# Performance work log

Measured on AMD Instinct MI355X. Metric: run time of the kernel, lower is better.

The kernel has to match this reference:

```python
import jax, jax.numpy as jnp
import numpy as np

B, T, D = 8, 4096, 64

def setup_inputs() -> dict:
    key = jax.random.key(0)
    k1, k2 = jax.random.split(key)
    inputs = jax.random.normal(k1, (B, T, D), dtype=jnp.float32)
    # keras 'random_normal' initializer: stddev 0.05
    W = jax.random.normal(k2, (D, D), dtype=jnp.float32) * 0.05
    return {"inputs": inputs, "W": W}

def reference(inputs, W):
    # q = inputs @ W               : [B,T,D]
    # a = q @ inputs^T             : [B,T,T] (no scaling, bias b unused in original)
    # out = softmax(a, -1) @ inputs: [B,T,D]
    q = jnp.einsum('btd,de->bte', inputs, W)
    scores = jnp.einsum('btd,bsd->bts', q, inputs)
    attn = jax.nn.softmax(scores, axis=-1)
    return jnp.einsum('bts,bsd->btd', attn, inputs)
```

## Files before the change

### kernel.cpp

```cpp
#include <hip/hip_runtime.h>

typedef _Float16 f16;
typedef _Float16 f16x8 __attribute__((ext_vector_type(8)));
typedef __bf16 bf16x8 __attribute__((ext_vector_type(8)));
typedef float floatx4 __attribute__((ext_vector_type(4)));
typedef unsigned short u16;
typedef unsigned int u32;

#define B_N   8
#define T_SEQ 4096
#define DIM   64
#define NIT   32
#define FRAG  512
#define XSTR  72
#define LOG2E 1.44269504f

#if __has_builtin(__builtin_amdgcn_exp2f)
#define EXP2(x) __builtin_amdgcn_exp2f(x)
#else
#define EXP2(x) exp2f(x)
#endif

__device__ __forceinline__ uint4 xpose(uint2 p0, uint2 p1, int qd, int ln) {
  const int pos = qd & 1;
  u32 mx = pos ? p1.x : p0.x, my = pos ? p1.y : p0.y;
  u32 ox = pos ? p0.x : p1.x, oy = pos ? p0.y : p1.y;
  u32 tx = (u32)__shfl_xor((int)ox, 16, 64);
  u32 ty = (u32)__shfl_xor((int)oy, 16, 64);
  u32 lox = pos ? tx : mx, loy = pos ? ty : my;
  u32 hix = pos ? mx : tx, hiy = pos ? my : ty;
  const int src = ((2 * pos + (qd >> 1)) << 4) | ln;
  uint4 r;
  r.x = (u32)__shfl((int)lox, src, 64);
  r.y = (u32)__shfl((int)loy, src, 64);
  r.z = (u32)__shfl((int)hix, src, 64);
  r.w = (u32)__shfl((int)hiy, src, 64);
  return r;
}

__device__ __forceinline__ uint2 pack_bf4(floatx4 v) {
  __bf16 b0 = (__bf16)v[0], b1 = (__bf16)v[1], b2 = (__bf16)v[2], b3 = (__bf16)v[3];
  uint2 r;
  r.x = ((u32)__builtin_bit_cast(u16, b1) << 16) | __builtin_bit_cast(u16, b0);
  r.y = ((u32)__builtin_bit_cast(u16, b3) << 16) | __builtin_bit_cast(u16, b2);
  return r;
}
__device__ __forceinline__ uint2 pack_f16x4(floatx4 v, float sc) {
  f16 b0 = (f16)(v[0] * sc), b1 = (f16)(v[1] * sc), b2 = (f16)(v[2] * sc), b3 = (f16)(v[3] * sc);
  uint2 r;
  r.x = ((u32)__builtin_bit_cast(u16, b1) << 16) | __builtin_bit_cast(u16, b0);
  r.y = ((u32)__builtin_bit_cast(u16, b3) << 16) | __builtin_bit_cast(u16, b2);
  return r;
}

__launch_bounds__(256, 2)
__global__ void prep_kernel(const float* __restrict__ X,
                            u16* __restrict__ Kswz, u16* __restrict__ Vswz) {
  __shared__ __attribute__((aligned(16))) u16 Xs[DIM * XSTR];
  const int tid = threadIdx.x;
  const int lane = tid & 63, w = tid >> 6, qd = lane >> 4, ln = lane & 15;
  const int b = blockIdx.y, tx = blockIdx.x;
  const long xbase = ((long)b * T_SEQ + tx * 64) * DIM;

  {
    const int r = tid >> 2, c0 = (tid & 3) * 16;
    float v[16];
#pragma unroll
    for (int i = 0; i < 4; i++)
      *(float4*)&v[i * 4] = *(const float4*)(X + xbase + (long)r * DIM + c0 + i * 4);
    u16 h[16];
#pragma unroll
    for (int j = 0; j < 16; j++) h[j] = __builtin_bit_cast(u16, (f16)v[j]);
    *(uint4*)&Xs[r * XSTR + c0] = *(uint4*)&h[0];
    *(uint4*)&Xs[r * XSTR + c0 + 8] = *(uint4*)&h[8];
  }
  __syncthreads();

  {
    const long R = (long)b * (T_SEQ / 16) + tx * 4 + w;
#pragma unroll
    for (int ks = 0; ks < 2; ks++) {
      f16x8 kv = *(const f16x8*)&Xs[(w * 16 + ln) * XSTR + ks * 32 + qd * 8];
      *(f16x8*)(Kswz + (R * 2 + ks) * FRAG + lane * 8) = kv;
    }
  }
  {
    const long Cb = (long)b * 4 + w;
#pragma unroll
    for (int J = 0; J < 2; J++) {
      bf16x8 vv;
#pragma unroll
      for (int j = 0; j < 8; j++) {
        f16 hv = __builtin_bit_cast(f16, Xs[(J * 32 + qd * 8 + j) * XSTR + w * 16 + ln]);
        vv[j] = (__bf16)(float)hv;
      }
      *(bf16x8*)(Vswz + (Cb * (T_SEQ / 32) + tx * 2 + J) * FRAG + lane * 8) = vv;
    }
  }
}

__launch_bounds__(512, 4)
__global__ void attn_kernel(const u16* __restrict__ Kswz, const u16* __restrict__ Vswz,
                            const float* __restrict__ W, float* __restrict__ out) {
  __shared__ __attribute__((aligned(16))) float Opart[8][16][68];
  __shared__ float lpart[8][32];

  const int tid = threadIdx.x;
  const int lane = tid & 63, w = tid >> 6, qd = lane >> 4, ln = lane & 15;
  const int h = w >> 2;
  const int s = w & 3;
  const int bid = blockIdx.x;
  const int b = bid & 7;
  const int q0 = (bid >> 3) * 64;
  const long bbase = (long)b * T_SEQ * DIM;
  const long RB = (long)b * (T_SEQ / 16);

  f16x8 bXq[2][2];
#pragma unroll
  for (int rb = 0; rb < 2; rb++)
#pragma unroll
    for (int ks = 0; ks < 2; ks++)
      bXq[rb][ks] = *(const f16x8*)(Kswz +
          ((RB + (q0 >> 4) + h * 2 + rb) * 2 + ks) * FRAG + lane * 8);

  floatx4 accT[4][2];
#pragma unroll
  for (int eb = 0; eb < 4; eb++)
#pragma unroll
    for (int rb = 0; rb < 2; rb++) accT[eb][rb] = (floatx4)0.0f;
#pragma unroll
  for (int ks = 0; ks < 2; ks++)
#pragma unroll
    for (int eb = 0; eb < 4; eb++) {
      f16 tw[8];
#pragma unroll
      for (int j = 0; j < 8; j++)
        tw[j] = (f16)W[(ks * 32 + qd * 8 + j) * DIM + eb * 16 + ln];
      f16x8 aW = *(const f16x8*)tw;
#pragma unroll
      for (int rb = 0; rb < 2; rb++)
        accT[eb][rb] = __builtin_amdgcn_mfma_f32_16x16x32_f16(aW, bXq[rb][ks], accT[eb][rb], 0, 0, 0);
    }

  f16x8 bQ[2][2];
#pragma unroll
  for (int rb = 0; rb < 2; rb++)
#pragma unroll
    for (int ks = 0; ks < 2; ks++) {
      uint2 p0 = pack_f16x4(accT[ks * 2 + 0][rb], LOG2E);
      uint2 p1 = pack_f16x4(accT[ks * 2 + 1][rb], LOG2E);
      uint4 t = xpose(p0, p1, qd, ln);
      bQ[rb][ks] = __builtin_bit_cast(f16x8, t);
    }

  floatx4 O[4][2];
  float lacc[2] = {0.f, 0.f};
#pragma unroll
  for (int db = 0; db < 4; db++)
#pragma unroll
    for (int rb = 0; rb < 2; rb++) O[db][rb] = (floatx4)0.0f;

  const u16* pK = Kswz + (RB + s * 2) * 2 * FRAG + lane * 8;
  const u16* pV = Vswz + ((long)(b * 4) * (T_SEQ / 32) + s) * FRAG + lane * 8;

#pragma unroll 1
  for (int kt = 0; kt < NIT; kt++) {
    f16x8 kc[2][2];
#pragma unroll
    for (int ct = 0; ct < 2; ct++)
#pragma unroll
      for (int ks = 0; ks < 2; ks++)
        kc[ct][ks] = *(const f16x8*)(pK + (long)(kt * 16 + ct * 2 + ks) * FRAG);
    bf16x8 aV[4];
#pragma unroll
    for (int db = 0; db < 4; db++)
      aV[db] = *(const bf16x8*)(pV + ((long)db * (T_SEQ / 32) + kt * 4) * FRAG);

    floatx4 St[2][2];
#pragma unroll
    for (int ct = 0; ct < 2; ct++)
#pragma unroll
      for (int rb = 0; rb < 2; rb++) St[ct][rb] = (floatx4)0.0f;
#pragma unroll
    for (int ks = 0; ks < 2; ks++)
#pragma unroll
      for (int ct = 0; ct < 2; ct++)
#pragma unroll
        for (int rb = 0; rb < 2; rb++)
          St[ct][rb] = __builtin_amdgcn_mfma_f32_16x16x32_f16(kc[ct][ks], bQ[rb][ks], St[ct][rb], 0, 0, 0);

    bf16x8 bP[2];
#pragma unroll
    for (int rb = 0; rb < 2; rb++) {
      floatx4 e0, e1;
      float ps = 0.f;
#pragma unroll
      for (int r = 0; r < 4; r++) { e0[r] = EXP2(St[0][rb][r]); ps += e0[r]; }
#pragma unroll
      for (int r = 0; r < 4; r++) { e1[r] = EXP2(St[1][rb][r]); ps += e1[r]; }
      lacc[rb] += ps;
      bP[rb] = __builtin_bit_cast(bf16x8, xpose(pack_bf4(e0), pack_bf4(e1), qd, ln));
    }

#pragma unroll
    for (int db = 0; db < 4; db++)
#pragma unroll
      for (int rb = 0; rb < 2; rb++)
        O[db][rb] = __builtin_amdgcn_mfma_f32_16x16x32_bf16(aV[db], bP[rb], O[db][rb], 0, 0, 0);
  }

#pragma unroll
  for (int rb = 0; rb < 2; rb++) {
    float v = lacc[rb];
    v += __shfl_xor(v, 16, 64);
    v += __shfl_xor(v, 32, 64);
    if (qd == 0) lpart[w][rb * 16 + ln] = v;
  }

#pragma unroll 1
  for (int rb = 0; rb < 2; rb++) {
    __syncthreads();
#pragma unroll
    for (int db = 0; db < 4; db++)
      *(float4*)&Opart[w][ln][db * 16 + qd * 4] = __builtin_bit_cast(float4, O[db][rb]);
    __syncthreads();
    const int hh = tid >> 8;
    const int ql = (tid >> 4) & 15;
    const int d4 = tid & 15;
    float4 a = {0.f, 0.f, 0.f, 0.f};
    float l = 0.f;
#pragma unroll
    for (int ss = 0; ss < 4; ss++) {
      const int ww = hh * 4 + ss;
      float4 p = *(const float4*)&Opart[ww][ql][d4 * 4];
      a.x += p.x; a.y += p.y; a.z += p.z; a.w += p.w;
      l += lpart[ww][rb * 16 + ql];
    }
    float inv = 1.0f / l;
    float4 o;
    o.x = a.x * inv; o.y = a.y * inv; o.z = a.z * inv; o.w = a.w * inv;
    *(float4*)(out + bbase + (long)(q0 + hh * 32 + rb * 16 + ql) * DIM + d4 * 4) = o;
  }
}

extern "C" void kernel_launch(void* const* d_in, const int* in_sizes, int n_in,
                              void* d_out, int out_size, void* d_ws, size_t ws_size,
                              hipStream_t stream) {
  const float* X = (const float*)d_in[0];
  const float* W = (const float*)d_in[1];
  float* out = (float*)d_out;
  const size_t SZ = (size_t)B_N * T_SEQ * DIM * 2;
  u16* Kswz = (u16*)d_ws;
  u16* Vswz = (u16*)((char*)d_ws + SZ);
  prep_kernel<<<dim3(T_SEQ / 64, B_N), 256, 0, stream>>>(X, Kswz, Vswz);
  attn_kernel<<<dim3(B_N * (T_SEQ / 64)), 512, 0, stream>>>(Kswz, Vswz, W, out);
}
```

Before: 125.5 us.

## Route softmax probabilities through LDS instead of cross-lane shuffles; drop prep LDS staging

```diff
diff --git a/kernel.cpp b/kernel.cpp
--- a/kernel.cpp
+++ b/kernel.cpp
@@ -12,7 +12,7 @@
 #define DIM   64
 #define NIT   32
 #define FRAG  512
-#define XSTR  72
+#define PSTR  40
 #define LOG2E 1.44269504f
 
 #if __has_builtin(__builtin_amdgcn_exp2f)
@@ -37,7 +37,6 @@
   r.w = (u32)__shfl((int)hiy, src, 64);
   return r;
 }
-
 __device__ __forceinline__ uint2 pack_bf4(floatx4 v) {
   __bf16 b0 = (__bf16)v[0], b1 = (__bf16)v[1], b2 = (__bf16)v[2], b3 = (__bf16)v[3];
   uint2 r;
@@ -53,35 +52,24 @@
   return r;
 }
 
-__launch_bounds__(256, 2)
+__launch_bounds__(256, 4)
 __global__ void prep_kernel(const float* __restrict__ X,
                             u16* __restrict__ Kswz, u16* __restrict__ Vswz) {
-  __shared__ __attribute__((aligned(16))) u16 Xs[DIM * XSTR];
   const int tid = threadIdx.x;
   const int lane = tid & 63, w = tid >> 6, qd = lane >> 4, ln = lane & 15;
   const int b = blockIdx.y, tx = blockIdx.x;
   const long xbase = ((long)b * T_SEQ + tx * 64) * DIM;
 
   {
-    const int r = tid >> 2, c0 = (tid & 3) * 16;
-    float v[16];
-#pragma unroll
-    for (int i = 0; i < 4; i++)
-      *(float4*)&v[i * 4] = *(const float4*)(X + xbase + (long)r * DIM + c0 + i * 4);
-    u16 h[16];
-#pragma unroll
-    for (int j = 0; j < 16; j++) h[j] = __builtin_bit_cast(u16, (f16)v[j]);
-    *(uint4*)&Xs[r * XSTR + c0] = *(uint4*)&h[0];
-    *(uint4*)&Xs[r * XSTR + c0 + 8] = *(uint4*)&h[8];
-  }
-  __syncthreads();
-
-  {
     const long R = (long)b * (T_SEQ / 16) + tx * 4 + w;
+    const float* src = X + xbase + (long)(w * 16 + ln) * DIM + qd * 8;
 #pragma unroll
     for (int ks = 0; ks < 2; ks++) {
-      f16x8 kv = *(const f16x8*)&Xs[(w * 16 + ln) * XSTR + ks * 32 + qd * 8];
-      *(f16x8*)(Kswz + (R * 2 + ks) * FRAG + lane * 8) = kv;
+      float4 a = *(const float4*)(src + ks * 32);
+      float4 c = *(const float4*)(src + ks * 32 + 4);
+      f16 h[8] = {(f16)a.x, (f16)a.y, (f16)a.z, (f16)a.w,
+                  (f16)c.x, (f16)c.y, (f16)c.z, (f16)c.w};
+      *(f16x8*)(Kswz + (R * 2 + ks) * FRAG + lane * 8) = *(const f16x8*)h;
     }
   }
   {
@@ -91,8 +79,8 @@
       bf16x8 vv;
 #pragma unroll
       for (int j = 0; j < 8; j++) {
-        f16 hv = __builtin_bit_cast(f16, Xs[(J * 32 + qd * 8 + j) * XSTR + w * 16 + ln]);
-        vv[j] = (__bf16)(float)hv;
+        float x = X[xbase + (long)(J * 32 + qd * 8 + j) * DIM + w * 16 + ln];
+        vv[j] = (__bf16)x;
       }
       *(bf16x8*)(Vswz + (Cb * (T_SEQ / 32) + tx * 2 + J) * FRAG + lane * 8) = vv;
     }
@@ -102,8 +90,11 @@
 __launch_bounds__(512, 4)
 __global__ void attn_kernel(const u16* __restrict__ Kswz, const u16* __restrict__ Vswz,
                             const float* __restrict__ W, float* __restrict__ out) {
-  __shared__ __attribute__((aligned(16))) float Opart[8][16][68];
+  __shared__ __attribute__((aligned(16))) char smem[8 * 16 * 68 * 4];
   __shared__ float lpart[8][32];
+
+  u16* Ps = (u16*)smem;
+  float* Opart = (float*)smem;
 
   const int tid = threadIdx.x;
   const int lane = tid & 63, w = tid >> 6, qd = lane >> 4, ln = lane & 15;
@@ -114,6 +105,7 @@
   const int q0 = (bid >> 3) * 64;
   const long bbase = (long)b * T_SEQ * DIM;
   const long RB = (long)b * (T_SEQ / 16);
+  u16* Pw = Ps + w * (32 * PSTR);
 
   f16x8 bXq[2][2];
 #pragma unroll
@@ -149,19 +141,18 @@
     for (int ks = 0; ks < 2; ks++) {
       uint2 p0 = pack_f16x4(accT[ks * 2 + 0][rb], LOG2E);
       uint2 p1 = pack_f16x4(accT[ks * 2 + 1][rb], LOG2E);
-      uint4 t = xpose(p0, p1, qd, ln);
-      bQ[rb][ks] = __builtin_bit_cast(f16x8, t);
-    }
-
-  floatx4 O[4][2];
+      bQ[rb][ks] = __builtin_bit_cast(f16x8, xpose(p0, p1, qd, ln));
+    }
+
+  floatx4 O[2][4];
   float lacc[2] = {0.f, 0.f};
 #pragma unroll
-  for (int db = 0; db < 4; db++)
-#pragma unroll
-    for (int rb = 0; rb < 2; rb++) O[db][rb] = (floatx4)0.0f;
+  for (int rb = 0; rb < 2; rb++)
+#pragma unroll
+    for (int cd = 0; cd < 4; cd++) O[rb][cd] = (floatx4)0.0f;
 
   const u16* pK = Kswz + (RB + s * 2) * 2 * FRAG + lane * 8;
-  const u16* pV = Vswz + ((long)(b * 4) * (T_SEQ / 32) + s) * FRAG + lane * 8;
+  const u16* pV = Vswz + ((long)b * 4 * (T_SEQ / 32) + s) * FRAG + lane * 8;
 
 #pragma unroll 1
   for (int kt = 0; kt < NIT; kt++) {
@@ -171,10 +162,10 @@
 #pragma unroll
       for (int ks = 0; ks < 2; ks++)
         kc[ct][ks] = *(const f16x8*)(pK + (long)(kt * 16 + ct * 2 + ks) * FRAG);
-    bf16x8 aV[4];
-#pragma unroll
-    for (int db = 0; db < 4; db++)
-      aV[db] = *(const bf16x8*)(pV + ((long)db * (T_SEQ / 32) + kt * 4) * FRAG);
+    bf16x8 bV[4];
+#pragma unroll
+    for (int cd = 0; cd < 4; cd++)
+      bV[cd] = *(const bf16x8*)(pV + ((long)cd * (T_SEQ / 32) + kt * 4) * FRAG);
 
     floatx4 St[2][2];
 #pragma unroll
@@ -189,24 +180,25 @@
         for (int rb = 0; rb < 2; rb++)
           St[ct][rb] = __builtin_amdgcn_mfma_f32_16x16x32_f16(kc[ct][ks], bQ[rb][ks], St[ct][rb], 0, 0, 0);
 
-    bf16x8 bP[2];
+#pragma unroll
+    for (int rb = 0; rb < 2; rb++)
+#pragma unroll
+      for (int ct = 0; ct < 2; ct++) {
+        floatx4 e;
+        float ps = 0.f;
+#pragma unroll
+        for (int r = 0; r < 4; r++) { e[r] = EXP2(St[ct][rb][r]); ps += e[r]; }
+        lacc[rb] += ps;
+        *(uint2*)&Pw[(rb * 16 + ln) * PSTR + ct * 16 + qd * 4] = pack_bf4(e);
+      }
+
 #pragma unroll
     for (int rb = 0; rb < 2; rb++) {
-      floatx4 e0, e1;
-      float ps = 0.f;
-#pragma unroll
-      for (int r = 0; r < 4; r++) { e0[r] = EXP2(St[0][rb][r]); ps += e0[r]; }
-#pragma unroll
-      for (int r = 0; r < 4; r++) { e1[r] = EXP2(St[1][rb][r]); ps += e1[r]; }
-      lacc[rb] += ps;
-      bP[rb] = __builtin_bit_cast(bf16x8, xpose(pack_bf4(e0), pack_bf4(e1), qd, ln));
-    }
-
-#pragma unroll
-    for (int db = 0; db < 4; db++)
-#pragma unroll
-      for (int rb = 0; rb < 2; rb++)
-        O[db][rb] = __builtin_amdgcn_mfma_f32_16x16x32_bf16(aV[db], bP[rb], O[db][rb], 0, 0, 0);
+      bf16x8 aP = *(const bf16x8*)&Pw[(rb * 16 + ln) * PSTR + qd * 8];
+#pragma unroll
+      for (int cd = 0; cd < 4; cd++)
+        O[rb][cd] = __builtin_amdgcn_mfma_f32_16x16x32_bf16(aP, bV[cd], O[rb][cd], 0, 0, 0);
+    }
   }
 
 #pragma unroll
@@ -221,8 +213,10 @@
   for (int rb = 0; rb < 2; rb++) {
     __syncthreads();
 #pragma unroll
-    for (int db = 0; db < 4; db++)
-      *(float4*)&Opart[w][ln][db * 16 + qd * 4] = __builtin_bit_cast(float4, O[db][rb]);
+    for (int cd = 0; cd < 4; cd++)
+#pragma unroll
+      for (int r = 0; r < 4; r++)
+        Opart[w * 16 * 68 + (qd * 4 + r) * 68 + cd * 16 + ln] = O[rb][cd][r];
     __syncthreads();
     const int hh = tid >> 8;
     const int ql = (tid >> 4) & 15;
@@ -232,7 +226,7 @@
 #pragma unroll
     for (int ss = 0; ss < 4; ss++) {
       const int ww = hh * 4 + ss;
-      float4 p = *(const float4*)&Opart[ww][ql][d4 * 4];
+      float4 p = *(const float4*)&Opart[ww * 16 * 68 + ql * 68 + d4 * 4];
       a.x += p.x; a.y += p.y; a.z += p.z; a.w += p.w;
       l += lpart[ww][rb * 16 + ql];
     }
```

Measured after the change: 124.5 us. About the same (-0.8%).
